# Kernel tuning notes

Measured on AMD Instinct MI355X. Metric: run time of the kernel, lower is better.

## Reference

```python
import jax, jax.numpy as jnp
import numpy as np
import math

B, N, DIM, NH, K, PD = 2, 2048, 512, 8, 32, 16
HD = DIM // NH
LN_EPS = 1e-6  # flax LayerNorm default


def _poincare_dist(x, y, c):
    # x, y broadcast to [B, N, N, PD]; returns [B, N, N]
    diff_norm_sq = jnp.sum((x - y) ** 2, axis=-1)
    x_norm_sq = jnp.sum(x ** 2, axis=-1)
    y_norm_sq = jnp.sum(y ** 2, axis=-1)
    den = (1.0 - c * x_norm_sq) * (1.0 - c * y_norm_sq)
    arg = 1.0 + 2.0 * c * diff_norm_sq / jnp.clip(den, 1e-8)
    safe_arg = jnp.maximum(arg, 1.0 + 1e-7)
    return jnp.arccosh(safe_arg) / jnp.sqrt(c)


def _layernorm(x, scale, bias):
    m = jnp.mean(x, axis=-1, keepdims=True)
    v = jnp.var(x, axis=-1, keepdims=True)
    return (x - m) / jnp.sqrt(v + LN_EPS) * scale + bias


def setup_inputs() -> dict:
    key = jax.random.key(0)
    ks = jax.random.split(key, 12)

    def dense(k, din, dout):
        W = jax.random.normal(k, (din, dout), jnp.float32) / np.sqrt(din).astype(np.float32)
        b = jnp.zeros((dout,), jnp.float32)
        return W, b

    inp = {}
    inp["x"] = jax.random.normal(ks[0], (B, N, DIM), jnp.float32)
    # points inside the unit Poincare ball (c=1)
    inp["positions"] = (jax.random.uniform(ks[1], (B, N, PD), jnp.float32) - 0.5) * 0.2
    inp["c"] = jnp.float32(1.0)
    inp["Wq"], inp["bq"] = dense(ks[2], DIM, DIM)
    inp["Wk"], inp["bk"] = dense(ks[3], DIM, DIM)
    inp["Wv"], inp["bv"] = dense(ks[4], DIM, DIM)
    inp["Wo"], inp["bo"] = dense(ks[5], DIM, DIM)
    inp["W1"], inp["b1"] = dense(ks[6], DIM, 4 * DIM)
    inp["W2"], inp["b2"] = dense(ks[7], 4 * DIM, DIM)
    inp["ln1_scale"] = jnp.ones((DIM,), jnp.float32)
    inp["ln1_bias"] = jnp.zeros((DIM,), jnp.float32)
    inp["ln2_scale"] = jnp.ones((DIM,), jnp.float32)
    inp["ln2_bias"] = jnp.zeros((DIM,), jnp.float32)
    inp["log_tau"] = jnp.zeros((1,), jnp.float32)
    inp["attn_scale"] = jnp.ones((1,), jnp.float32)
    return inp


def reference(x, positions, c, Wq, bq, Wk, bk, Wv, bv, Wo, bo,
              W1, b1, W2, b2, ln1_scale, ln1_bias, ln2_scale, ln2_bias,
              log_tau, attn_scale):
    x_res = x
    x_norm = _layernorm(x, ln1_scale, ln1_bias)

    def heads(W, b):
        return (x_norm @ W + b).reshape(B, N, NH, HD).transpose(0, 2, 1, 3)  # [B,H,N,HD]

    q = heads(Wq, bq)
    k = heads(Wk, bk)
    v = heads(Wv, bv)

    # pairwise hyperbolic distances [B,N,N]
    dist_matrix = _poincare_dist(positions[:, None, :, :], positions[:, :, None, :], c)
    _, top_k_indices = jax.lax.top_k(-dist_matrix, K)  # [B,N,K]

    # gather neighbor K/V: out[b,h,i,j,d] = kv[b,h, idx[b,i,j], d]
    gather = jax.vmap(lambda kv_b, idx_b: kv_b[:, idx_b, :])
    k_gathered = gather(k, top_k_indices)  # [B,H,N,K,HD]
    v_gathered = gather(v, top_k_indices)  # [B,H,N,K,HD]

    feature_scores = jnp.einsum('bhid,bhikd->bhik', q, k_gathered) / math.sqrt(HD)
    gathered_dists = jnp.take_along_axis(dist_matrix, top_k_indices, axis=-1)  # [B,N,K]
    geometric_scores = -gathered_dists[:, None, :, :] / jnp.clip(jnp.exp(log_tau), 1e-8)
    attn_scores = attn_scale * jnp.tanh(feature_scores + geometric_scores)
    attn_weights = jax.nn.softmax(attn_scores, axis=-1)

    attn_output = jnp.einsum('bhik,bhikd->bhid', attn_weights, v_gathered)
    attn_output = attn_output.transpose(0, 2, 1, 3).reshape(B, N, DIM)

    x1 = x_res + attn_output @ Wo + bo
    x2_norm = _layernorm(x1, ln2_scale, ln2_bias)
    ffn = jax.nn.gelu(x2_norm @ W1 + b1) @ W2 + b2  # gelu approximate=True (flax default)
    return x1 + ffn
```

## Files before the change

### kernel.cpp

```cpp
#include <hip/hip_runtime.h>
#include <math.h>

#define B_   2
#define N_   2048
#define DIM_ 512
#define NH_  8
#define HD_  64
#define K_   32
#define PD_  16
#define TOK_ (B_*N_)
#define FFN_ 2048
#define QKV_ (3*DIM_)
#define KV_  1024

typedef __bf16 bf16x8 __attribute__((ext_vector_type(8)));
typedef float  f32x4  __attribute__((ext_vector_type(4)));

__device__ __forceinline__ unsigned short f2bf(float f) {
    unsigned int u = __float_as_uint(f);
    u = (u + 0x7fffu + ((u >> 16) & 1u)) >> 16;
    return (unsigned short)u;
}

__device__ __forceinline__ float bflo(unsigned u) { return __uint_as_float(u << 16); }
__device__ __forceinline__ float bfhi(unsigned u) { return __uint_as_float(u & 0xffff0000u); }

__device__ __forceinline__ float gelu_tanh(float x) {
    float x3 = x * x * x;
    return 0.5f * x * (1.f + tanhf(0.7978845608028654f * (x + 0.044715f * x3)));
}

__device__ __forceinline__ float tanh_fast(float x) {
    float e = __expf(2.f * x);
    return 1.f - 2.f / (e + 1.f);
}

__device__ __forceinline__ int lane_mbcnt(unsigned long long m) {
    return __builtin_amdgcn_mbcnt_hi((unsigned)(m >> 32),
           __builtin_amdgcn_mbcnt_lo((unsigned)m, 0));
}

#define GLOAD_LDS16(g, l) __builtin_amdgcn_global_load_lds(                        \
    (const __attribute__((address_space(1))) unsigned int*)(const void*)(g),       \
    (__attribute__((address_space(3))) unsigned int*)(void*)(l), 16, 0, 0)

template<int EPI, int BM, int BN, bool DBUF>
__device__ __forceinline__ void gemm_block(const unsigned short* __restrict__ A,
                      const unsigned short* __restrict__ Bt,
                      const float* __restrict__ bias,
                      const float* __restrict__ res,
                      float* __restrict__ Cf,
                      unsigned short* __restrict__ Cb,
                      int N, int Kd, int bm0, int bn0,
                      unsigned short* smem)
{
    constexpr int WM = BM / 2;
    constexpr int WN = BN / 2;
    constexpr int FM = WM / 16;
    constexpr int FN = WN / 16;
    constexpr int BUFSZ = (BM + BN) * 64;

    int t    = threadIdx.x;
    int lane = t & 63;
    int wid  = t >> 6;
    int wm   = wid >> 1, wn = wid & 1;
    int quad = lane >> 4;
    int rlo  = lane & 15;

    f32x4 acc[FM][FN] = {};

    auto stage = [&](int buf, int k0) {
        unsigned short* As_ = smem + buf * BUFSZ;
        unsigned short* Bs_ = As_ + BM * 64;
#pragma unroll
        for (int l = 0; l < BM/32; l++) {
            int idx = l*256 + t;
            int r   = idx >> 3;
            int g   = (idx & 7) ^ (r & 7);
            GLOAD_LDS16(A + (size_t)(bm0 + r) * Kd + k0 + g*8, As_ + idx*8);
        }
#pragma unroll
        for (int l = 0; l < BN/32; l++) {
            int idx = l*256 + t;
            int r   = idx >> 3;
            int g   = (idx & 7) ^ (r & 7);
            GLOAD_LDS16(Bt + (size_t)(bn0 + r) * Kd + k0 + g*8, Bs_ + idx*8);
        }
    };

    auto compute = [&](int buf) {
        unsigned short* As_ = smem + buf * BUFSZ;
        unsigned short* Bs_ = As_ + BM * 64;
        bf16x8 af[FM][2], bfr[FN][2];
#pragma unroll
        for (int mi = 0; mi < FM; mi++) {
            int r = wm*WM + mi*16 + rlo;
#pragma unroll
            for (int s = 0; s < 2; s++)
                af[mi][s] = *(const bf16x8*)(As_ + r*64 + ((s*4 + quad) ^ (r & 7))*8);
        }
#pragma unroll
        for (int ni = 0; ni < FN; ni++) {
            int r = wn*WN + ni*16 + rlo;
#pragma unroll
            for (int s = 0; s < 2; s++)
                bfr[ni][s] = *(const bf16x8*)(Bs_ + r*64 + ((s*4 + quad) ^ (r & 7))*8);
        }
#pragma unroll
        for (int s = 0; s < 2; s++)
#pragma unroll
            for (int mi = 0; mi < FM; mi++)
#pragma unroll
                for (int ni = 0; ni < FN; ni++)
                    acc[mi][ni] = __builtin_amdgcn_mfma_f32_16x16x32_bf16(
                        af[mi][s], bfr[ni][s], acc[mi][ni], 0, 0, 0);
    };

    if constexpr (DBUF) {
        stage(0, 0);
        int buf = 0;
        for (int k0 = 0; k0 < Kd; k0 += 64) {
            __syncthreads();
            if (k0 + 64 < Kd) stage(buf ^ 1, k0 + 64);
            compute(buf);
            buf ^= 1;
        }
    } else {
        for (int k0 = 0; k0 < Kd; k0 += 64) {
            stage(0, k0);
            __syncthreads();
            compute(0);
            __syncthreads();
        }
    }

#pragma unroll
    for (int mi = 0; mi < FM; mi++) {
#pragma unroll
        for (int ni = 0; ni < FN; ni++) {
            int col = bn0 + wn*WN + ni*16 + rlo;
            float bv = bias[col];
#pragma unroll
            for (int r = 0; r < 4; r++) {
                int row = bm0 + wm*WM + mi*16 + quad*4 + r;
                float val = acc[mi][ni][r] + bv;
                if (EPI == 1) val += res[(size_t)row * N + col];
                if (EPI == 2) {
                    val = gelu_tanh(val);
                    Cb[(size_t)row * N + col] = f2bf(val);
                } else if (EPI == 3) {
                    if (col < DIM_) Cf[(size_t)row * DIM_ + col] = val;
                    else            Cb[(size_t)row * KV_ + (col - DIM_)] = f2bf(val);
                } else {
                    Cf[(size_t)row * N + col] = val;
                }
            }
        }
    }
}

template<int EPI, int BM, int BN>
__global__ __launch_bounds__(256)
void gemm_bf16_kernel(const unsigned short* __restrict__ A,
                      const unsigned short* __restrict__ Bt,
                      const float* __restrict__ bias,
                      const float* __restrict__ res,
                      float* __restrict__ Cf,
                      unsigned short* __restrict__ Cb,
                      int N, int Kd)
{
    __shared__ __align__(16) unsigned short smem[2 * (BM + BN) * 64];
    gemm_block<EPI, BM, BN, true>(A, Bt, bias, res, Cf, Cb, N, Kd,
                                  blockIdx.y * BM, blockIdx.x * BN, smem);
}

template<int NR>
__device__ __forceinline__ void extract_row(const unsigned* rb, unsigned T,
                                            int cnt_lt, int m,
                                            unsigned long long* crow,
                                            int part, int jbase, int lane)
{
    int ltpos = 0;
#pragma unroll
    for (int tt = 0; tt < NR; tt++) {
        bool is_lt = rb[tt] < T;
        unsigned long long mlt = __ballot(is_lt);
        int p = ltpos + lane_mbcnt(mlt);
        if (is_lt) {
            int j = jbase + (tt >> 2)*256 + lane*4 + (tt & 3);
            crow[part*K_ + p] = ((unsigned long long)rb[tt] << 32) | (unsigned)j;
        }
        ltpos += __popcll(mlt);
    }
    int eqpos = 0;
#pragma unroll
    for (int jg = 0; jg < NR/4; jg++) {
        bool iseq[4]; unsigned long long meq[4]; int bel[4];
#pragma unroll
        for (int jj = 0; jj < 4; jj++) {
            iseq[jj] = (rb[jg*4+jj] == T);
            meq[jj]  = __ballot(iseq[jj]);
            bel[jj]  = lane_mbcnt(meq[jj]);
        }
        int lane_prefix = bel[0] + bel[1] + bel[2] + bel[3];
        int within = 0;
#pragma unroll
        for (int jj = 0; jj < 4; jj++) {
            int p = eqpos + lane_prefix + within;
            if (iseq[jj] && p < m) {
                int j = jbase + jg*256 + lane*4 + jj;
                crow[part*K_ + cnt_lt + p] =
                    ((unsigned long long)rb[jg*4+jj] << 32) | (unsigned)j;
            }
            within += iseq[jj] ? 1 : 0;
        }
        eqpos += __popcll(meq[0]) + __popcll(meq[1]) + __popcll(meq[2]) + __popcll(meq[3]);
    }
}

__device__ __forceinline__ void topk_block(const float* __restrict__ pos,
                      const float* __restrict__ posT,
                      const float* __restrict__ pos_sq,
                      const float* __restrict__ c_ptr,
                      int* __restrict__ topk_idx, float* __restrict__ topk_dist,
                      int bi0, unsigned long long (*cand)[128])
{
    int wid  = threadIdx.x >> 6;
    int lane = threadIdx.x & 63;
    int b    = bi0 >> 11;
    float c  = *c_ptr;
    float inv_sqrt_c = rsqrtf(c);

    float pi0[16], pi1[16];
    {
        const float4* q0 = (const float4*)(pos + (size_t)bi0 * PD_);
        const float4* q1 = (const float4*)(pos + (size_t)(bi0+1) * PD_);
#pragma unroll
        for (int u = 0; u < 4; u++) {
            float4 a = q0[u];
            pi0[4*u]=a.x; pi0[4*u+1]=a.y; pi0[4*u+2]=a.z; pi0[4*u+3]=a.w;
            float4 e = q1[u];
            pi1[4*u]=e.x; pi1[4*u+1]=e.y; pi1[4*u+2]=e.z; pi1[4*u+3]=e.w;
        }
    }
    float om0 = 1.f - c * pos_sq[bi0];
    float om1 = 1.f - c * pos_sq[bi0+1];

    const float* pT  = posT + (size_t)b * 16 * N_;
    const float* sqb = pos_sq + b * N_;
    int jbase = wid * 512;
    int j0l   = jbase + lane * 4;

    unsigned rb0[8], rb1[8];
#pragma unroll
    for (int jg = 0; jg < 2; jg++) {
        int j0 = j0l + jg * 256;
        float ax=0,ay=0,az=0,aw=0, bx=0,by=0,bz=0,bw=0;
#pragma unroll
        for (int d = 0; d < 16; d++) {
            float4 v = *(const float4*)(pT + d * N_ + j0);
            float d0x = pi0[d]-v.x, d0y = pi0[d]-v.y, d0z = pi0[d]-v.z, d0w = pi0[d]-v.w;
            ax += d0x*d0x; ay += d0y*d0y; az += d0z*d0z; aw += d0w*d0w;
            float d1x = pi1[d]-v.x, d1y = pi1[d]-v.y, d1z = pi1[d]-v.z, d1w = pi1[d]-v.w;
            bx += d1x*d1x; by += d1y*d1y; bz += d1z*d1z; bw += d1w*d1w;
        }
        float4 sq = *(const float4*)(sqb + j0);
        float da[4]={ax,ay,az,aw}, db[4]={bx,by,bz,bw}, sqa[4]={sq.x,sq.y,sq.z,sq.w};
#pragma unroll
        for (int jj = 0; jj < 4; jj++) {
            float omj  = 1.f - c * sqa[jj];
            float den0 = fmaxf(om0 * omj, 1e-8f);
            float den1 = fmaxf(om1 * omj, 1e-8f);
            rb0[jg*4+jj] = __float_as_uint(fmaxf(1.f + 2.f*c*da[jj]/den0, 1.f+1e-7f));
            rb1[jg*4+jj] = __float_as_uint(fmaxf(1.f + 2.f*c*db[jj]/den1, 1.f+1e-7f));
        }
    }

    unsigned T0, T1;
    int cl0 = 0, cl1 = 0;
    {
        unsigned band0 = rb0[0], bor0 = rb0[0], band1 = rb1[0], bor1 = rb1[0];
#pragma unroll
        for (int tt = 1; tt < 8; tt++) {
            band0 &= rb0[tt]; bor0 |= rb0[tt];
            band1 &= rb1[tt]; bor1 |= rb1[tt];
        }
#pragma unroll
        for (int off = 32; off; off >>= 1) {
            band0 &= __shfl_xor(band0, off); bor0 |= __shfl_xor(bor0, off);
            band1 &= __shfl_xor(band1, off); bor1 |= __shfl_xor(bor1, off);
        }
        unsigned df0 = band0 ^ bor0, df1 = band1 ^ bor1;
        int hib0 = df0 ? (31 - __clz(df0)) : -1;
        int hib1 = df1 ? (31 - __clz(df1)) : -1;
        int hib  = hib0 > hib1 ? hib0 : hib1;
        T0 = (hib >= 0) ? (band0 & ~((1u << (hib+1)) - 1u)) : band0;
        T1 = (hib >= 0) ? (band1 & ~((1u << (hib+1)) - 1u)) : band1;
        int bit = hib;
        while (bit >= 1) {
            unsigned lo = 1u << (bit - 1);
            unsigned p01 = T0 | lo, p02 = T0 | (lo << 1), p03 = T0 | (lo*3u);
            unsigned p11 = T1 | lo, p12 = T1 | (lo << 1), p13 = T1 | (lo*3u);
            int c01=0,c02=0,c03=0,c11=0,c12=0,c13=0;
#pragma unroll
            for (int tt = 0; tt < 8; tt++) {
                c01 += __popcll(__ballot(rb0[tt] < p01));
                c02 += __popcll(__ballot(rb0[tt] < p02));
                c03 += __popcll(__ballot(rb0[tt] < p03));
                c11 += __popcll(__ballot(rb1[tt] < p11));
                c12 += __popcll(__ballot(rb1[tt] < p12));
                c13 += __popcll(__ballot(rb1[tt] < p13));
            }
            if      (c03 < K_) { T0 = p03; cl0 = c03; }
            else if (c02 < K_) { T0 = p02; cl0 = c02; }
            else if (c01 < K_) { T0 = p01; cl0 = c01; }
            if      (c13 < K_) { T1 = p13; cl1 = c13; }
            else if (c12 < K_) { T1 = p12; cl1 = c12; }
            else if (c11 < K_) { T1 = p11; cl1 = c11; }
            bit -= 2;
        }
        if (bit == 0) {
            unsigned p0 = T0 | 1u, p1 = T1 | 1u;
            int c0 = 0, c1 = 0;
#pragma unroll
            for (int tt = 0; tt < 8; tt++) {
                c0 += __popcll(__ballot(rb0[tt] < p0));
                c1 += __popcll(__ballot(rb1[tt] < p1));
            }
            if (c0 < K_) { T0 = p0; cl0 = c0; }
            if (c1 < K_) { T1 = p1; cl1 = c1; }
        }
    }

    extract_row<8>(rb0, T0, cl0, K_ - cl0, cand[0], wid, jbase, lane);
    extract_row<8>(rb1, T1, cl1, K_ - cl1, cand[1], wid, jbase, lane);
    __syncthreads();

    {
        int row  = wid >> 1, half = wid & 1;
        unsigned long long mykey = cand[row][half*64 + lane];
        int rank = 0;
#pragma unroll 8
        for (int M = 0; M < 128; M++)
            rank += (cand[row][M] < mykey) ? 1 : 0;
        if (rank < K_) {
            int bi = bi0 + row;
            topk_idx [(size_t)bi * K_ + rank] = (int)(mykey & 0xffffffffu);
            topk_dist[(size_t)bi * K_ + rank] =
                acoshf(__uint_as_float((unsigned)(mykey >> 32))) * inv_sqrt_c;
        }
    }
}

__global__ __launch_bounds__(256)
void qkv_topk_kernel(const unsigned short* __restrict__ xn,
                     const unsigned short* __restrict__ qkvWt,
                     const float* __restrict__ qkv_b,
                     float* __restrict__ qf,
                     unsigned short* __restrict__ kvb,
                     const float* __restrict__ pos,
                     const float* __restrict__ posT,
                     const float* __restrict__ pos_sq,
                     const float* __restrict__ c_ptr,
                     int* __restrict__ tk_i, float* __restrict__ tk_d,
                     const float* __restrict__ Wo, const float* __restrict__ W1,
                     const float* __restrict__ W2,
                     unsigned short* __restrict__ WoT,
                     unsigned short* __restrict__ W1T,
                     unsigned short* __restrict__ W2T)
{
    __shared__ __align__(16) unsigned short smem[(64 + 64) * 64];

    int g = blockIdx.x;
    int grp = g / 23;
    int r   = g - grp * 23;
    if (r < 6) {
        int gb = grp * 6 + r;
        int bx = gb % 24, by = gb / 24;
        gemm_block<3, 64, 64, false>(xn, qkvWt, qkv_b, nullptr, qf, kvb, QKV_, DIM_,
                                     by * 64, bx * 64, smem);
    } else if (r < 14) {
        int tb = grp * 8 + (r - 6);
        topk_block(pos, posT, pos_sq, c_ptr, tk_i, tk_d, tb * 2,
                   (unsigned long long (*)[128])smem);
    } else {
        int tid = grp * 9 + (r - 14);
        const float* W; unsigned short* Wt; int Kd, Nw, nx, ti;
        if      (tid < 256)  { W = Wo; Wt = WoT; Kd = 512;  Nw = 512;  nx = 16; ti = tid; }
        else if (tid < 1280) { W = W1; Wt = W1T; Kd = 512;  Nw = 2048; nx = 64; ti = tid - 256; }
        else                 { W = W2; Wt = W2T; Kd = 2048; Nw = 512;  nx = 16; ti = tid - 1280; }
        float (*tile)[33] = (float (*)[33])smem;
        int t  = threadIdx.x;
        int n0 = (ti % nx) * 32, k0 = (ti / nx) * 32;
        int tx = t & 31, ty = t >> 5;
#pragma unroll
        for (int i = 0; i < 32; i += 8)
            tile[ty + i][tx] = W[(size_t)(k0 + ty + i) * Nw + n0 + tx];
        __syncthreads();
#pragma unroll
        for (int i = 0; i < 32; i += 8)
            Wt[(size_t)(n0 + ty + i) * Kd + k0 + tx] = f2bf(tile[tx][ty + i]);
    }
}

__global__ void fused_prep_kernel(const float* __restrict__ Wq, const float* __restrict__ Wk,
                            const float* __restrict__ Wv,
                            const float* __restrict__ bq, const float* __restrict__ bk,
                            const float* __restrict__ bv,
                            unsigned short* __restrict__ qkvWt,
                            float* __restrict__ qkv_b,
                            const float* __restrict__ pos,
                            float* __restrict__ pos_sq,
                            float* __restrict__ posT,
                            const float* __restrict__ x,
                            const float* __restrict__ ln1_scale,
                            const float* __restrict__ ln1_bias,
                            unsigned short* __restrict__ xn)
{
    int id = blockIdx.x;
    int t  = threadIdx.x;

    if (id >= 790) {
        int wave = (id - 790) * 4 + (t >> 6);
        int lane = t & 63;
        const float* xr = x + (size_t)wave * DIM_;
        float v[8];
        float s = 0.f;
#pragma unroll
        for (int i = 0; i < 8; i++) { v[i] = xr[lane + i*64]; s += v[i]; }
#pragma unroll
        for (int off = 32; off; off >>= 1) s += __shfl_xor(s, off);
        float mean = s * (1.f / DIM_);
        float vs = 0.f;
#pragma unroll
        for (int i = 0; i < 8; i++) { float d = v[i] - mean; vs += d*d; }
#pragma unroll
        for (int off = 32; off; off >>= 1) vs += __shfl_xor(vs, off);
        float inv = rsqrtf(vs * (1.f / DIM_) + 1e-6f);
        unsigned short* yr = xn + (size_t)wave * DIM_;
#pragma unroll
        for (int i = 0; i < 8; i++) {
            int cc = lane + i*64;
            yr[cc] = f2bf((v[i] - mean) * inv * ln1_scale[cc] + ln1_bias[cc]);
        }
        return;
    }
    if (id >= 774) {
        int i = (id - 774) * 256 + t;
        int b = i >> 11, j = i & (N_ - 1);
        const float4* p = (const float4*)(pos + (size_t)i * PD_);
        float4 a0 = p[0], a1 = p[1], a2 = p[2], a3 = p[3];
        float pv[16] = {a0.x,a0.y,a0.z,a0.w, a1.x,a1.y,a1.z,a1.w,
                        a2.x,a2.y,a2.z,a2.w, a3.x,a3.y,a3.z,a3.w};
        float s = 0.f;
#pragma unroll
        for (int d = 0; d < 16; d++) s += pv[d]*pv[d];
        pos_sq[i] = s;
        float* pT = posT + (size_t)b * 16 * N_;
#pragma unroll
        for (int d = 0; d < 16; d++) pT[d * N_ + j] = pv[d];
        return;
    }
    if (id >= 768) {
        int i = (id - 768) * 256 + t;
        if (i < DIM_)            qkv_b[i] = bq[i];
        else if (i < 2*DIM_)     qkv_b[i] = bk[i - DIM_];
        else                     qkv_b[i] = bv[i - 2*DIM_];
        return;
    }

    const float* W; unsigned short* Wt; int ti;
    if      (id < 256)  { W = Wq; Wt = qkvWt;             ti = id; }
    else if (id < 512)  { W = Wk; Wt = qkvWt + 512*512;   ti = id - 256; }
    else                { W = Wv; Wt = qkvWt + 2*512*512; ti = id - 512; }

    __shared__ float tile[32][33];
    int n0 = (ti % 16) * 32, k0 = (ti / 16) * 32;
    int tx = t & 31, ty = t >> 5;
#pragma unroll
    for (int i = 0; i < 32; i += 8)
        tile[ty + i][tx] = W[(size_t)(k0 + ty + i) * 512 + n0 + tx];
    __syncthreads();
#pragma unroll
    for (int i = 0; i < 32; i += 8)
        Wt[(size_t)(n0 + ty + i) * 512 + k0 + tx] = f2bf(tile[tx][ty + i]);
}

__global__ void layernorm_kernel(const float* __restrict__ x,
                                 const float* __restrict__ scale,
                                 const float* __restrict__ bias,
                                 unsigned short* __restrict__ y)
{
    int wave = (blockIdx.x * blockDim.x + threadIdx.x) >> 6;
    int lane = threadIdx.x & 63;
    if (wave >= TOK_) return;
    const float* xr = x + (size_t)wave * DIM_;
    float v[8];
    float s = 0.f;
#pragma unroll
    for (int i = 0; i < 8; i++) { v[i] = xr[lane + i*64]; s += v[i]; }
#pragma unroll
    for (int off = 32; off; off >>= 1) s += __shfl_xor(s, off);
    float mean = s * (1.f / DIM_);
    float vs = 0.f;
#pragma unroll
    for (int i = 0; i < 8; i++) { float d = v[i] - mean; vs += d*d; }
#pragma unroll
    for (int off = 32; off; off >>= 1) vs += __shfl_xor(vs, off);
    float inv = rsqrtf(vs * (1.f / DIM_) + 1e-6f);
    unsigned short* yr = y + (size_t)wave * DIM_;
#pragma unroll
    for (int i = 0; i < 8; i++) {
        int c = lane + i*64;
        yr[c] = f2bf((v[i] - mean) * inv * scale[c] + bias[c]);
    }
}

__global__ __launch_bounds__(256)
void attn_kernel(const float* __restrict__ q,
                 const unsigned short* __restrict__ kv,
                 const int* __restrict__ topk_idx, const float* __restrict__ topk_dist,
                 const float* __restrict__ log_tau_p, const float* __restrict__ attn_scale_p,
                 unsigned int* __restrict__ out)
{
    int gw   = (blockIdx.x * blockDim.x + threadIdx.x) >> 6;
    int lane = threadIdx.x & 63;
    if (gw >= B_ * NH_ * N_) return;
    int b = gw / (NH_ * N_);
    int r = gw % (NH_ * N_);
    int h = r / N_;
    int i = r % N_;
    int tok = b * N_ + i;

    float tau    = fmaxf(__expf(*log_tau_p), 1e-8f);
    float ascale = *attn_scale_p;

    const int*   idxp = topk_idx  + (size_t)tok * K_;
    const float* dstp = topk_dist + (size_t)tok * K_;
    int   my_idx  = idxp[lane & 31];
    float my_dist = dstp[lane & 31];

    int jj   = lane >> 1;
    int half = lane & 1;

    const float4* qp = (const float4*)(q + (size_t)tok * DIM_ + h * HD_ + half * 32);
    float4 qv[8];
#pragma unroll
    for (int u = 0; u < 8; u++) qv[u] = qp[u];

    int nb = __shfl(my_idx, jj);
    const uint4* kp = (const uint4*)(kv + (size_t)(b * N_ + nb) * KV_ + h * HD_ + half * 32);
    float dot = 0.f;
#pragma unroll
    for (int u = 0; u < 4; u++) {
        uint4 kw = kp[u];
        dot += qv[2*u].x   * bflo(kw.x) + qv[2*u].y   * bfhi(kw.x)
             + qv[2*u].z   * bflo(kw.y) + qv[2*u].w   * bfhi(kw.y)
             + qv[2*u+1].x * bflo(kw.z) + qv[2*u+1].y * bfhi(kw.z)
             + qv[2*u+1].z * bflo(kw.w) + qv[2*u+1].w * bfhi(kw.w);
    }
    dot += __shfl_xor(dot, 1);

    float fs = dot * 0.125f;
    float gs = -__shfl(my_dist, jj) / tau;
    float s  = ascale * tanh_fast(fs + gs);

    float mx = s;
#pragma unroll
    for (int off = 32; off; off >>= 1) mx = fmaxf(mx, __shfl_xor(mx, off));
    float e  = __expf(s - mx);
    float ec = half ? 0.f : e;
#pragma unroll
    for (int off = 32; off; off >>= 1) ec += __shfl_xor(ec, off);
    float inv = 1.f / ec;

    int dp    = lane & 31;
    int half2 = lane >> 5;
    const unsigned int* vb = (const unsigned int*)(kv + DIM_ + h * HD_) + dp;
    float ax = 0.f, ay = 0.f;
#pragma unroll
    for (int it = 0; it < 16; it++) {
        int t2 = half2 + 2*it;
        float w  = __shfl(e, t2 * 2) * inv;
        int   nj = __shfl(my_idx, t2);
        unsigned vv = vb[(size_t)(b * N_ + nj) * (KV_/2)];
        ax += w * bflo(vv);
        ay += w * bfhi(vv);
    }
    ax += __shfl_xor(ax, 32);
    ay += __shfl_xor(ay, 32);
    if (lane < 32) {
        unsigned pck = ((unsigned)f2bf(ay) << 16) | (unsigned)f2bf(ax);
        out[(size_t)tok * (DIM_/2) + h * (HD_/2) + dp] = pck;
    }
}

extern "C" void kernel_launch(void* const* d_in, const int* in_sizes, int n_in,
                              void* d_out, int out_size, void* d_ws, size_t ws_size,
                              hipStream_t stream)
{
    const float* x          = (const float*)d_in[0];
    const float* positions  = (const float*)d_in[1];
    const float* c_p        = (const float*)d_in[2];
    const float* Wq         = (const float*)d_in[3];
    const float* bq         = (const float*)d_in[4];
    const float* Wk         = (const float*)d_in[5];
    const float* bk         = (const float*)d_in[6];
    const float* Wv         = (const float*)d_in[7];
    const float* bv         = (const float*)d_in[8];
    const float* Wo         = (const float*)d_in[9];
    const float* bo         = (const float*)d_in[10];
    const float* W1         = (const float*)d_in[11];
    const float* b1         = (const float*)d_in[12];
    const float* W2         = (const float*)d_in[13];
    const float* b2         = (const float*)d_in[14];
    const float* ln1_scale  = (const float*)d_in[15];
    const float* ln1_bias   = (const float*)d_in[16];
    const float* ln2_scale  = (const float*)d_in[17];
    const float* ln2_bias   = (const float*)d_in[18];
    const float* log_tau    = (const float*)d_in[19];
    const float* attn_scale = (const float*)d_in[20];

    char* p = (char*)d_ws;
    unsigned short* qkvWt  = (unsigned short*)p; p += (size_t)QKV_ * DIM_ * 2;
    unsigned short* WoT    = (unsigned short*)p; p += (size_t)DIM_ * DIM_ * 2;
    unsigned short* W1T    = (unsigned short*)p; p += (size_t)FFN_ * DIM_ * 2;
    unsigned short* W2T    = (unsigned short*)p; p += (size_t)DIM_ * FFN_ * 2;
    float*          qkv_b  = (float*)p;          p += (size_t)QKV_ * 4;
    unsigned short* xn     = (unsigned short*)p; p += (size_t)TOK_ * DIM_ * 2;
    float*          qf     = (float*)p;          p += (size_t)TOK_ * DIM_ * 4;
    unsigned short* kvb    = (unsigned short*)p; p += (size_t)TOK_ * KV_ * 2;
    unsigned short* attn_o = (unsigned short*)p; p += (size_t)TOK_ * DIM_ * 2;
    float*          x1     = (float*)p;          p += (size_t)TOK_ * DIM_ * 4;
    unsigned short* x2n    = (unsigned short*)p; p += (size_t)TOK_ * DIM_ * 2;
    unsigned short* hbuf   = (unsigned short*)p; p += (size_t)TOK_ * FFN_ * 2;
    float*          pos_sq = (float*)p;          p += (size_t)TOK_ * 4;
    float*          posT   = (float*)p;          p += (size_t)B_ * 16 * N_ * 4;
    float*          tk_d   = (float*)p;          p += (size_t)TOK_ * K_ * 4;
    int*            tk_i   = (int*)p;            p += (size_t)TOK_ * K_ * 4;

    fused_prep_kernel<<<1814, 256, 0, stream>>>(Wq, Wk, Wv, bq, bk, bv,
                                                qkvWt, qkv_b,
                                                positions, pos_sq, posT,
                                                x, ln1_scale, ln1_bias, xn);

    qkv_topk_kernel<<<5888, 256, 0, stream>>>(xn, qkvWt, qkv_b, qf, kvb,
                                              positions, posT, pos_sq, c_p,
                                              tk_i, tk_d,
                                              Wo, W1, W2, WoT, W1T, W2T);

    attn_kernel<<<(B_*NH_*N_)/4, 256, 0, stream>>>(qf, kvb, tk_i, tk_d,
                                                   log_tau, attn_scale,
                                                   (unsigned int*)attn_o);

    gemm_bf16_kernel<1,64,64><<<dim3(DIM_/64, TOK_/64), 256, 0, stream>>>(
        attn_o, WoT, bo, x, x1, nullptr, DIM_, DIM_);

    layernorm_kernel<<<TOK_/4, 256, 0, stream>>>(x1, ln2_scale, ln2_bias, x2n);

    gemm_bf16_kernel<2,128,128><<<dim3(FFN_/128, TOK_/128), 256, 0, stream>>>(
        x2n, W1T, b1, nullptr, nullptr, hbuf, FFN_, DIM_);

    gemm_bf16_kernel<1,64,64><<<dim3(DIM_/64, TOK_/64), 256, 0, stream>>>(
        hbuf, W2T, b2, x1, (float*)d_out, nullptr, DIM_, FFN_);
}
```

Baseline: 243.4 us.

## Fuse second LayerNorm into Wo-GEMM stats and FFN1 A-tile staging

Removes the standalone LayerNorm kernel. The Wo projection epilogue now accumulates per-row sum and sum of squares with atomics into a stats buffer, which is zeroed by two extra blocks in the prep kernel. A new FFN1 kernel reads fp32 x1 and applies the normalization while staging the A tile into LDS as bf16. This saves one launch and the x2n round trip. In exchange, FFN1 reads fp32 A data through registers instead of async LDS loads, re-normalizes the same rows once per column block, and computes variance as E[x^2]-m^2, which loses some precision.

```diff
diff --git a/kernel.cpp b/kernel.cpp
--- a/kernel.cpp
+++ b/kernel.cpp
@@ -52,7 +52,9 @@
                       float* __restrict__ Cf,
                       unsigned short* __restrict__ Cb,
                       int N, int Kd, int bm0, int bn0,
-                      unsigned short* smem)
+                      unsigned short* smem,
+                      float* __restrict__ su = nullptr,
+                      float* __restrict__ sq = nullptr)
 {
     constexpr int WM = BM / 2;
     constexpr int WN = BN / 2;
@@ -134,6 +136,13 @@
         }
     }
 
+    float rs_[FM][4], rq_[FM][4];
+    if (EPI == 4) {
+#pragma unroll
+        for (int mi = 0; mi < FM; mi++)
+#pragma unroll
+            for (int r = 0; r < 4; r++) { rs_[mi][r] = 0.f; rq_[mi][r] = 0.f; }
+    }
 #pragma unroll
     for (int mi = 0; mi < FM; mi++) {
 #pragma unroll
@@ -144,7 +153,7 @@
             for (int r = 0; r < 4; r++) {
                 int row = bm0 + wm*WM + mi*16 + quad*4 + r;
                 float val = acc[mi][ni][r] + bv;
-                if (EPI == 1) val += res[(size_t)row * N + col];
+                if (EPI == 1 || EPI == 4) val += res[(size_t)row * N + col];
                 if (EPI == 2) {
                     val = gelu_tanh(val);
                     Cb[(size_t)row * N + col] = f2bf(val);
@@ -154,6 +163,26 @@
                 } else {
                     Cf[(size_t)row * N + col] = val;
                 }
+                if (EPI == 4) { rs_[mi][r] += val; rq_[mi][r] += val * val; }
+            }
+        }
+    }
+    if (EPI == 4) {
+#pragma unroll
+        for (int mi = 0; mi < FM; mi++) {
+#pragma unroll
+            for (int r = 0; r < 4; r++) {
+                float s_ = rs_[mi][r], q_ = rq_[mi][r];
+#pragma unroll
+                for (int off = 1; off < 16; off <<= 1) {
+                    s_ += __shfl_xor(s_, off);
+                    q_ += __shfl_xor(q_, off);
+                }
+                if (rlo == 0) {
+                    int row = bm0 + wm*WM + mi*16 + quad*4 + r;
+                    atomicAdd(&su[row], s_);
+                    atomicAdd(&sq[row], q_);
+                }
             }
         }
     }
@@ -167,11 +196,137 @@
                       const float* __restrict__ res,
                       float* __restrict__ Cf,
                       unsigned short* __restrict__ Cb,
-                      int N, int Kd)
+                      int N, int Kd,
+                      float* __restrict__ su, float* __restrict__ sq)
 {
     __shared__ __align__(16) unsigned short smem[2 * (BM + BN) * 64];
     gemm_block<EPI, BM, BN, true>(A, Bt, bias, res, Cf, Cb, N, Kd,
-                                  blockIdx.y * BM, blockIdx.x * BN, smem);
+                                  blockIdx.y * BM, blockIdx.x * BN, smem, su, sq);
+}
+
+__global__ __launch_bounds__(256)
+void ffn1_ln_kernel(const float* __restrict__ x1,
+                    const unsigned short* __restrict__ W1T,
+                    const float* __restrict__ bias1,
+                    const float* __restrict__ su, const float* __restrict__ sq,
+                    const float* __restrict__ lsc, const float* __restrict__ lbi,
+                    unsigned short* __restrict__ hb)
+{
+    constexpr int BM = 128, BN = 128;
+    constexpr int BUFSZ = (BM + BN) * 64;
+    __shared__ __align__(16) unsigned short smem[2 * BUFSZ];
+
+    int t    = threadIdx.x;
+    int lane = t & 63;
+    int wid  = t >> 6;
+    int wm   = wid >> 1, wn = wid & 1;
+    int quad = lane >> 4;
+    int rlo  = lane & 15;
+    int bm0  = blockIdx.y * BM;
+    int bn0  = blockIdx.x * BN;
+
+    float nm_[4], rstd_[4];
+#pragma unroll
+    for (int l = 0; l < 4; l++) {
+        int r   = (l*256 + t) >> 3;
+        int row = bm0 + r;
+        float m = su[row] * (1.f / DIM_);
+        float v = sq[row] * (1.f / DIM_) - m * m;
+        nm_[l]   = m;
+        rstd_[l] = rsqrtf(v + 1e-6f);
+    }
+
+    f32x4 acc[4][4] = {};
+
+    auto stageA = [&](int buf, int k0) {
+        unsigned short* As_ = smem + buf * BUFSZ;
+#pragma unroll
+        for (int l = 0; l < 4; l++) {
+            int idx = l*256 + t;
+            int r   = idx >> 3;
+            int g   = (idx & 7) ^ (r & 7);
+            int c0  = k0 + g*8;
+            const float* xr = x1 + (size_t)(bm0 + r) * DIM_ + c0;
+            float4 a  = *(const float4*)xr;
+            float4 bq = *(const float4*)(xr + 4);
+            float4 g0 = *(const float4*)(lsc + c0);
+            float4 g1 = *(const float4*)(lsc + c0 + 4);
+            float4 e0 = *(const float4*)(lbi + c0);
+            float4 e1 = *(const float4*)(lbi + c0 + 4);
+            float m = nm_[l], rs = rstd_[l];
+            unsigned w0 = (unsigned)f2bf((a.x - m)*rs*g0.x + e0.x)
+                        | ((unsigned)f2bf((a.y - m)*rs*g0.y + e0.y) << 16);
+            unsigned w1 = (unsigned)f2bf((a.z - m)*rs*g0.z + e0.z)
+                        | ((unsigned)f2bf((a.w - m)*rs*g0.w + e0.w) << 16);
+            unsigned w2 = (unsigned)f2bf((bq.x - m)*rs*g1.x + e1.x)
+                        | ((unsigned)f2bf((bq.y - m)*rs*g1.y + e1.y) << 16);
+            unsigned w3 = (unsigned)f2bf((bq.z - m)*rs*g1.z + e1.z)
+                        | ((unsigned)f2bf((bq.w - m)*rs*g1.w + e1.w) << 16);
+            uint4 pk = {w0, w1, w2, w3};
+            *(uint4*)(As_ + idx*8) = pk;
+        }
+    };
+    auto stageB = [&](int buf, int k0) {
+        unsigned short* Bs_ = smem + buf * BUFSZ + BM * 64;
+#pragma unroll
+        for (int l = 0; l < 4; l++) {
+            int idx = l*256 + t;
+            int r   = idx >> 3;
+            int g   = (idx & 7) ^ (r & 7);
+            GLOAD_LDS16(W1T + (size_t)(bn0 + r) * DIM_ + k0 + g*8, Bs_ + idx*8);
+        }
+    };
+    auto compute = [&](int buf) {
+        unsigned short* As_ = smem + buf * BUFSZ;
+        unsigned short* Bs_ = As_ + BM * 64;
+        bf16x8 af[4][2], bfr[4][2];
+#pragma unroll
+        for (int mi = 0; mi < 4; mi++) {
+            int r = wm*64 + mi*16 + rlo;
+#pragma unroll
+            for (int s = 0; s < 2; s++)
+                af[mi][s] = *(const bf16x8*)(As_ + r*64 + ((s*4 + quad) ^ (r & 7))*8);
+        }
+#pragma unroll
+        for (int ni = 0; ni < 4; ni++) {
+            int r = wn*64 + ni*16 + rlo;
+#pragma unroll
+            for (int s = 0; s < 2; s++)
+                bfr[ni][s] = *(const bf16x8*)(Bs_ + r*64 + ((s*4 + quad) ^ (r & 7))*8);
+        }
+#pragma unroll
+        for (int s = 0; s < 2; s++)
+#pragma unroll
+            for (int mi = 0; mi < 4; mi++)
+#pragma unroll
+                for (int ni = 0; ni < 4; ni++)
+                    acc[mi][ni] = __builtin_amdgcn_mfma_f32_16x16x32_bf16(
+                        af[mi][s], bfr[ni][s], acc[mi][ni], 0, 0, 0);
+    };
+
+    stageA(0, 0); stageB(0, 0);
+    int buf = 0;
+    for (int k0 = 0; k0 < DIM_; k0 += 64) {
+        __syncthreads();
+        if (k0 + 64 < DIM_) { stageA(buf ^ 1, k0 + 64); stageB(buf ^ 1, k0 + 64); }
+        compute(buf);
+        buf ^= 1;
+    }
+
+#pragma unroll
+    for (int mi = 0; mi < 4; mi++) {
+#pragma unroll
+        for (int ni = 0; ni < 4; ni++) {
+            int col = bn0 + wn*64 + ni*16 + rlo;
+            float bv = bias1[col];
+#pragma unroll
+            for (int r = 0; r < 4; r++) {
+                int row = bm0 + wm*64 + mi*16 + quad*4 + r;
+                float val = gelu_tanh(acc[mi][ni][r] + bv);
+                hb[(size_t)row * FFN_ + col] = f2bf(val);
+            }
+        }
+    }
 }
 
 template<int NR>
@@ -415,11 +570,20 @@
                             const float* __restrict__ x,
                             const float* __restrict__ ln1_scale,
                             const float* __restrict__ ln1_bias,
-                            unsigned short* __restrict__ xn)
+                            unsigned short* __restrict__ xn,
+                            float* __restrict__ lnstats)
 {
     int id = blockIdx.x;
     int t  = threadIdx.x;
 
+    if (id >= 1814) {
+        int i = (id - 1814) * 256 + t;
+        float4 z = {0.f, 0.f, 0.f, 0.f};
+        float4* dst = (float4*)(lnstats) + i * 4;
+#pragma unroll
+        for (int k = 0; k < 4; k++) dst[k] = z;
+        return;
+    }
     if (id >= 790) {
         int wave = (id - 790) * 4 + (t >> 6);
         int lane = t & 63;
@@ -484,36 +648,6 @@
 #pragma unroll
     for (int i = 0; i < 32; i += 8)
         Wt[(size_t)(n0 + ty + i) * 512 + k0 + tx] = f2bf(tile[tx][ty + i]);
-}
-
-__global__ void layernorm_kernel(const float* __restrict__ x,
-                                 const float* __restrict__ scale,
-                                 const float* __restrict__ bias,
-                                 unsigned short* __restrict__ y)
-{
-    int wave = (blockIdx.x * blockDim.x + threadIdx.x) >> 6;
-    int lane = threadIdx.x & 63;
-    if (wave >= TOK_) return;
-    const float* xr = x + (size_t)wave * DIM_;
-    float v[8];
-    float s = 0.f;
-#pragma unroll
-    for (int i = 0; i < 8; i++) { v[i] = xr[lane + i*64]; s += v[i]; }
-#pragma unroll
-    for (int off = 32; off; off >>= 1) s += __shfl_xor(s, off);
-    float mean = s * (1.f / DIM_);
-    float vs = 0.f;
-#pragma unroll
-    for (int i = 0; i < 8; i++) { float d = v[i] - mean; vs += d*d; }
-#pragma unroll
-    for (int off = 32; off; off >>= 1) vs += __shfl_xor(vs, off);
-    float inv = rsqrtf(vs * (1.f / DIM_) + 1e-6f);
-    unsigned short* yr = y + (size_t)wave * DIM_;
-#pragma unroll
-    for (int i = 0; i < 8; i++) {
-        int c = lane + i*64;
-        yr[c] = f2bf((v[i] - mean) * inv * scale[c] + bias[c]);
-    }
 }
 
 __global__ __launch_bounds__(256)
@@ -632,17 +766,18 @@
     unsigned short* kvb    = (unsigned short*)p; p += (size_t)TOK_ * KV_ * 2;
     unsigned short* attn_o = (unsigned short*)p; p += (size_t)TOK_ * DIM_ * 2;
     float*          x1     = (float*)p;          p += (size_t)TOK_ * DIM_ * 4;
-    unsigned short* x2n    = (unsigned short*)p; p += (size_t)TOK_ * DIM_ * 2;
+    float*          lnstat = (float*)p;          p += (size_t)2 * TOK_ * 4;
     unsigned short* hbuf   = (unsigned short*)p; p += (size_t)TOK_ * FFN_ * 2;
     float*          pos_sq = (float*)p;          p += (size_t)TOK_ * 4;
     float*          posT   = (float*)p;          p += (size_t)B_ * 16 * N_ * 4;
     float*          tk_d   = (float*)p;          p += (size_t)TOK_ * K_ * 4;
     int*            tk_i   = (int*)p;            p += (size_t)TOK_ * K_ * 4;
 
-    fused_prep_kernel<<<1814, 256, 0, stream>>>(Wq, Wk, Wv, bq, bk, bv,
+    fused_prep_kernel<<<1816, 256, 0, stream>>>(Wq, Wk, Wv, bq, bk, bv,
                                                 qkvWt, qkv_b,
                                                 positions, pos_sq, posT,
-                                                x, ln1_scale, ln1_bias, xn);
+                                                x, ln1_scale, ln1_bias, xn,
+                                                lnstat);
 
     qkv_topk_kernel<<<5888, 256, 0, stream>>>(xn, qkvWt, qkv_b, qf, kvb,
                                               positions, posT, pos_sq, c_p,
@@ -653,14 +788,12 @@
                                                    log_tau, attn_scale,
                                                    (unsigned int*)attn_o);
 
+    gemm_bf16_kernel<4,64,64><<<dim3(DIM_/64, TOK_/64), 256, 0, stream>>>(
+        attn_o, WoT, bo, x, x1, nullptr, DIM_, DIM_, lnstat, lnstat + TOK_);
+
+    ffn1_ln_kernel<<<dim3(FFN_/128, TOK_/128), 256, 0, stream>>>(
+        x1, W1T, b1, lnstat, lnstat + TOK_, ln2_scale, ln2_bias, hbuf);
+
     gemm_bf16_kernel<1,64,64><<<dim3(DIM_/64, TOK_/64), 256, 0, stream>>>(
-        attn_o, WoT, bo, x, x1, nullptr, DIM_, DIM_);
-
-    layernorm_kernel<<<TOK_/4, 256, 0, stream>>>(x1, ln2_scale, ln2_bias, x2n);
-
-    gemm_bf16_kernel<2,128,128><<<dim3(FFN_/128, TOK_/128), 256, 0, stream>>>(
-        x2n, W1T, b1, nullptr, nullptr, hbuf, FFN_, DIM_);
-
-    gemm_bf16_kernel<1,64,64><<<dim3(DIM_/64, TOK_/64), 256, 0, stream>>>(
-        hbuf, W2T, b2, x1, (float*)d_out, nullptr, DIM_, FFN_);
-}
+        hbuf, W2T, b2, x1, (float*)d_out, nullptr, DIM_, FFN_, nullptr, nullptr);
+}
```

After: 252.9 us. 1.04x slower.
